# Kernel tuning notes

Hardware: AMD Instinct MI355X
Metric: run time of the kernel (lower is better)

## Reference

```python
import jax, jax.numpy as jnp
import numpy as np

B, MN, GN, ME, GE = 1, 40962, 65160, 327660, 163848
MEMB = EEMB = 256
H1, H2 = 512, 64
EPS = 1e-5


def setup_inputs() -> dict:
    key = jax.random.key(0)
    ks = jax.random.split(key, 16)
    s = 0.05
    return {
        "gx": jax.random.normal(ks[0], (B, GN, MEMB), jnp.float32),
        "mx": jax.random.normal(ks[1], (B, MN, MEMB), jnp.float32),
        "me_i": jax.random.randint(ks[2], (2, ME), 0, MN),
        "me_x": jax.random.normal(ks[3], (B, ME, EEMB), jnp.float32),
        "g2me_i": jax.random.randint(ks[4], (2, GE), 0, MN),
        "g2me_x": jax.random.normal(ks[5], (B, GE, EEMB), jnp.float32),
        "m2ge_i": jax.random.randint(ks[6], (2, GE), 0, MN),
        "m2ge_x": jax.random.normal(ks[7], (B, GE, EEMB), jnp.float32),
        # learned params (Linear stored as [in, out]; y = x @ W + b, math-equivalent to torch)
        "W1": jax.random.normal(ks[8], (2 * MEMB + EEMB, H1), jnp.float32) * s,
        "b1": jnp.zeros((H1,), jnp.float32),
        "W2": jax.random.normal(ks[9], (H1, H2), jnp.float32) * s,
        "b2": jnp.zeros((H2,), jnp.float32),
        "W3": jax.random.normal(ks[10], (H2, EEMB), jnp.float32) * s,
        "b3": jnp.zeros((EEMB,), jnp.float32),
        # LayerNorm([m_enum, eemb]) -> elementwise affine over last two dims
        "ln_w": jnp.ones((ME, EEMB), jnp.float32),
        "ln_b": jnp.zeros((ME, EEMB), jnp.float32),
    }


def reference(gx, mx, me_i, me_x, g2me_i, g2me_x, m2ge_i, m2ge_x,
              W1, b1, W2, b2, W3, b3, ln_w, ln_b):
    row, col = me_i[0], me_i[1]
    # gather sender/receiver mesh-node features per edge: [B, ME, 2*MEMB+EEMB]
    h = jnp.concatenate([mx[:, row], mx[:, col], me_x], axis=-1)
    h = jax.nn.silu(h @ W1 + b1)
    h = jax.nn.silu(h @ W2 + b2)
    h = h @ W3 + b3
    # LayerNorm over the last TWO dims (m_enum, eemb), as nn.LayerNorm([m_enum, eemb])
    mean = jnp.mean(h, axis=(-2, -1), keepdims=True)
    var = jnp.var(h, axis=(-2, -1), keepdims=True)
    h = (h - mean) * jax.lax.rsqrt(var + EPS) * ln_w + ln_b
    me_x_new = me_x + h
    return (gx, mx, me_i, me_x_new, g2me_i, g2me_x, m2ge_i, m2ge_x)
```

## Files before the change

### kernel.cpp

```cpp
#include <hip/hip_runtime.h>
#include <hip/hip_bf16.h>

typedef unsigned short u16;
typedef unsigned int u32;
typedef __attribute__((ext_vector_type(8))) short bfrag8;
typedef __attribute__((ext_vector_type(4))) float f32x4;

#define ME_N 327660
#define MEMB_N 256
#define H1_N 512
#define H2_N 64
#define EEMB_N 256
#define LN_EPS 1e-5f
#define NBLK 5120

static __device__ __forceinline__ u16 f2bf(float f) {
  __hip_bfloat16 h = __float2bfloat16(f);
  return *reinterpret_cast<u16*>(&h);
}
static __device__ __forceinline__ float bf2f(u16 u) {
  union { u32 i; float f; } x; x.i = ((u32)u) << 16; return x.f;
}
static __device__ __forceinline__ u32 pack2(float a, float b) {
  return (u32)f2bf(a) | ((u32)f2bf(b) << 16);
}
static __device__ __forceinline__ float silu_f(float x) {
  return x / (1.0f + __expf(-x));
}
static __device__ __forceinline__ void gload_lds16(const void* g, void* l) {
  __builtin_amdgcn_global_load_lds(
      (const __attribute__((address_space(1))) void*)g,
      (__attribute__((address_space(3))) void*)l, 16, 0, 0);
}

__global__ void i2f_kernel(const int* __restrict__ src, float* __restrict__ dst, int n) {
  int i = blockIdx.x * 256 + threadIdx.x;
  if (i < n) dst[i] = (float)src[i];
}

__global__ void wconv_kernel(const float* __restrict__ src, u16* __restrict__ dst,
                             int K, int N) {
  int i = blockIdx.x * 256 + threadIdx.x;
  if (i >= K * N) return;
  int n = i / K;
  int k = i - n * K;
  dst[i] = f2bf(src[(size_t)k * N + n]);
}

__launch_bounds__(256, 2)
__global__ void gemm_fused_kernel(const float* __restrict__ mx, const int* __restrict__ me_i,
                                  const float* __restrict__ me_x,
                                  const u16* __restrict__ w1t, const float* __restrict__ b1,
                                  const u16* __restrict__ w2t, const float* __restrict__ b2,
                                  const u16* __restrict__ w3t, const float* __restrict__ b3,
                                  u16* __restrict__ h3, float* __restrict__ partials) {
  __shared__ u16 Alds[64 * 72];
  __shared__ u16 Blds[64 * 520];
  __shared__ float red[8];

  const int t = threadIdx.x;
  const int m0 = blockIdx.x * 64;
  const int lane = t & 63;
  const int wid = t >> 6;
  const int l16 = lane & 15;
  const int k4 = lane >> 4;

  const int arow = t >> 2;
  const int acol = (t & 3) * 16;
  int m_g = m0 + arow; if (m_g > ME_N - 1) m_g = ME_N - 1;
  const float* rp = mx + (size_t)me_i[m_g] * MEMB_N;
  const float* cp = mx + (size_t)me_i[ME_N + m_g] * MEMB_N;
  const float* ep = me_x + (size_t)m_g * EEMB_N;

  const f32x4 zero = {0.f, 0.f, 0.f, 0.f};
  f32x4 acc[4][8];
#pragma unroll
  for (int i = 0; i < 4; ++i)
#pragma unroll
    for (int j = 0; j < 8; ++j) acc[i][j] = zero;

  for (int kc = 0; kc < 12; ++kc) {
    const u16* bsrc = w1t + kc * 64 + (lane & 7) * 8;
#pragma unroll
    for (int q = 0; q < 16; ++q) {
      const int nbase = wid * 128 + q * 8;
      gload_lds16(bsrc + (size_t)(nbase + (lane >> 3)) * 768, &Blds[nbase * 64]);
    }
    const float* p = (kc < 4 ? rp : (kc < 8 ? cp : ep)) + ((kc & 3) * 64 + acol);
    const float4* p4 = reinterpret_cast<const float4*>(p);
    float4 v0 = p4[0], v1 = p4[1], v2 = p4[2], v3 = p4[3];
    uint4 q0, q1;
    q0.x = pack2(v0.x, v0.y); q0.y = pack2(v0.z, v0.w);
    q0.z = pack2(v1.x, v1.y); q0.w = pack2(v1.z, v1.w);
    q1.x = pack2(v2.x, v2.y); q1.y = pack2(v2.z, v2.w);
    q1.z = pack2(v3.x, v3.y); q1.w = pack2(v3.z, v3.w);
    *reinterpret_cast<uint4*>(&Alds[arow * 72 + acol]) = q0;
    *reinterpret_cast<uint4*>(&Alds[arow * 72 + acol + 8]) = q1;
    __syncthreads();
#pragma unroll
    for (int ks = 0; ks < 2; ++ks) {
      bfrag8 a[4], b[8];
#pragma unroll
      for (int i = 0; i < 4; ++i)
        a[i] = *reinterpret_cast<const bfrag8*>(&Alds[(i * 16 + l16) * 72 + ks * 32 + k4 * 8]);
#pragma unroll
      for (int j = 0; j < 8; ++j)
        b[j] = *reinterpret_cast<const bfrag8*>(&Blds[(wid * 128 + j * 16 + l16) * 64 + ks * 32 + k4 * 8]);
#pragma unroll
      for (int i = 0; i < 4; ++i)
#pragma unroll
        for (int j = 0; j < 8; ++j)
          acc[i][j] = __builtin_amdgcn_mfma_f32_16x16x32_bf16(a[i], b[j], acc[i][j], 0, 0, 0);
    }
    __syncthreads();
  }

  float b1v[8];
#pragma unroll
  for (int j = 0; j < 8; ++j) b1v[j] = b1[wid * 128 + j * 16 + l16];
#pragma unroll
  for (int i = 0; i < 4; ++i)
#pragma unroll
    for (int j = 0; j < 8; ++j)
#pragma unroll
      for (int rg = 0; rg < 4; ++rg) {
        float v = silu_f(acc[i][j][rg] + b1v[j]);
        Blds[(i * 16 + k4 * 4 + rg) * 520 + wid * 128 + j * 16 + l16] = f2bf(v);
      }
  __syncthreads();

  const int n2 = wid * 16 + l16;
  bfrag8 w2f[16];
#pragma unroll
  for (int ks = 0; ks < 16; ++ks)
    w2f[ks] = *reinterpret_cast<const bfrag8*>(w2t + (size_t)n2 * 512 + ks * 32 + k4 * 8);
  f32x4 acc2[4];
#pragma unroll
  for (int i = 0; i < 4; ++i) acc2[i] = zero;
#pragma unroll
  for (int ks = 0; ks < 16; ++ks) {
#pragma unroll
    for (int i = 0; i < 4; ++i) {
      bfrag8 a2 = *reinterpret_cast<const bfrag8*>(&Blds[(i * 16 + l16) * 520 + ks * 32 + k4 * 8]);
      acc2[i] = __builtin_amdgcn_mfma_f32_16x16x32_bf16(a2, w2f[ks], acc2[i], 0, 0, 0);
    }
  }
  const float b2v = b2[n2];
#pragma unroll
  for (int i = 0; i < 4; ++i)
#pragma unroll
    for (int rg = 0; rg < 4; ++rg) {
      float v = silu_f(acc2[i][rg] + b2v);
      Alds[(i * 16 + k4 * 4 + rg) * 72 + n2] = f2bf(v);
    }
  __syncthreads();

  bfrag8 w3f[4][2];
#pragma unroll
  for (int j = 0; j < 4; ++j)
#pragma unroll
    for (int ks = 0; ks < 2; ++ks)
      w3f[j][ks] = *reinterpret_cast<const bfrag8*>(
          w3t + (size_t)(wid * 64 + j * 16 + l16) * 64 + ks * 32 + k4 * 8);
  f32x4 acc3[4][4];
#pragma unroll
  for (int i = 0; i < 4; ++i)
#pragma unroll
    for (int j = 0; j < 4; ++j) acc3[i][j] = zero;
#pragma unroll
  for (int ks = 0; ks < 2; ++ks) {
    bfrag8 a3[4];
#pragma unroll
    for (int i = 0; i < 4; ++i)
      a3[i] = *reinterpret_cast<const bfrag8*>(&Alds[(i * 16 + l16) * 72 + ks * 32 + k4 * 8]);
#pragma unroll
    for (int i = 0; i < 4; ++i)
#pragma unroll
      for (int j = 0; j < 4; ++j)
        acc3[i][j] = __builtin_amdgcn_mfma_f32_16x16x32_bf16(a3[i], w3f[j][ks], acc3[i][j], 0, 0, 0);
  }

  float b3v[4];
#pragma unroll
  for (int j = 0; j < 4; ++j) b3v[j] = b3[wid * 64 + j * 16 + l16];
  float lsum = 0.f, lsq = 0.f;
#pragma unroll
  for (int i = 0; i < 4; ++i)
#pragma unroll
    for (int rg = 0; rg < 4; ++rg) {
      int m = m0 + i * 16 + k4 * 4 + rg;
      if (m < ME_N) {
#pragma unroll
        for (int j = 0; j < 4; ++j) {
          float v = acc3[i][j][rg] + b3v[j];
          h3[(size_t)m * EEMB_N + wid * 64 + j * 16 + l16] = f2bf(v);
          lsum += v;
          lsq += v * v;
        }
      }
    }
#pragma unroll
  for (int o = 32; o > 0; o >>= 1) {
    lsum += __shfl_down(lsum, o, 64);
    lsq  += __shfl_down(lsq, o, 64);
  }
  if (lane == 0) { red[wid] = lsum; red[4 + wid] = lsq; }
  __syncthreads();
  if (t == 0) {
    partials[2 * blockIdx.x]     = red[0] + red[1] + red[2] + red[3];
    partials[2 * blockIdx.x + 1] = red[4] + red[5] + red[6] + red[7];
  }
}

__global__ void reduce_kernel(const float* __restrict__ partials, int n,
                              float* __restrict__ stats) {
  __shared__ float s1[256], s2[256];
  float a = 0.f, b = 0.f;
  for (int i = threadIdx.x; i < n; i += 256) { a += partials[2 * i]; b += partials[2 * i + 1]; }
  s1[threadIdx.x] = a; s2[threadIdx.x] = b;
  __syncthreads();
  for (int off = 128; off > 0; off >>= 1) {
    if ((int)threadIdx.x < off) {
      s1[threadIdx.x] += s1[threadIdx.x + off];
      s2[threadIdx.x] += s2[threadIdx.x + off];
    }
    __syncthreads();
  }
  if (threadIdx.x == 0) {
    double cnt = (double)ME_N * (double)EEMB_N;
    double mean = (double)s1[0] / cnt;
    double var = (double)s2[0] / cnt - mean * mean;
    stats[0] = (float)mean;
    stats[1] = (float)(1.0 / sqrt(var + (double)LN_EPS));
  }
}

__launch_bounds__(256)
__global__ void final_kernel(const u16* __restrict__ h3, const float* __restrict__ me_x,
                             const float* __restrict__ ln_w, const float* __restrict__ ln_b,
                             const float* __restrict__ stats, float* __restrict__ out) {
  const size_t total = (size_t)ME_N * EEMB_N;
  size_t i = ((size_t)blockIdx.x * 256 + threadIdx.x) * 8;
  if (i >= total) return;
  const float mean = stats[0], inv = stats[1];
  uint4 hv = *reinterpret_cast<const uint4*>(h3 + i);
  float h[8];
  h[0] = bf2f((u16)(hv.x & 0xffff)); h[1] = bf2f((u16)(hv.x >> 16));
  h[2] = bf2f((u16)(hv.y & 0xffff)); h[3] = bf2f((u16)(hv.y >> 16));
  h[4] = bf2f((u16)(hv.z & 0xffff)); h[5] = bf2f((u16)(hv.z >> 16));
  h[6] = bf2f((u16)(hv.w & 0xffff)); h[7] = bf2f((u16)(hv.w >> 16));
  float4 m0 = reinterpret_cast<const float4*>(me_x + i)[0];
  float4 m1 = reinterpret_cast<const float4*>(me_x + i)[1];
  float4 w0 = reinterpret_cast<const float4*>(ln_w + i)[0];
  float4 w1 = reinterpret_cast<const float4*>(ln_w + i)[1];
  float4 c0 = reinterpret_cast<const float4*>(ln_b + i)[0];
  float4 c1 = reinterpret_cast<const float4*>(ln_b + i)[1];
  float4 o0, o1;
  o0.x = m0.x + (h[0] - mean) * inv * w0.x + c0.x;
  o0.y = m0.y + (h[1] - mean) * inv * w0.y + c0.y;
  o0.z = m0.z + (h[2] - mean) * inv * w0.z + c0.z;
  o0.w = m0.w + (h[3] - mean) * inv * w0.w + c0.w;
  o1.x = m1.x + (h[4] - mean) * inv * w1.x + c1.x;
  o1.y = m1.y + (h[5] - mean) * inv * w1.y + c1.y;
  o1.z = m1.z + (h[6] - mean) * inv * w1.z + c1.z;
  o1.w = m1.w + (h[7] - mean) * inv * w1.w + c1.w;
  reinterpret_cast<float4*>(out + i)[0] = o0;
  reinterpret_cast<float4*>(out + i)[1] = o1;
}

extern "C" void kernel_launch(void* const* d_in, const int* in_sizes, int n_in,
                              void* d_out, int out_size, void* d_ws, size_t ws_size,
                              hipStream_t stream) {
  const float* mx   = (const float*)d_in[1];
  const int*   me_i = (const int*)d_in[2];
  const float* me_x = (const float*)d_in[3];
  const float* W1 = (const float*)d_in[8];
  const float* b1 = (const float*)d_in[9];
  const float* W2 = (const float*)d_in[10];
  const float* b2 = (const float*)d_in[11];
  const float* W3 = (const float*)d_in[12];
  const float* b3 = (const float*)d_in[13];
  const float* ln_w = (const float*)d_in[14];
  const float* ln_b = (const float*)d_in[15];

  char* ws = (char*)d_ws;
  u16* w1t = (u16*)(ws + 0);
  u16* w2t = (u16*)(ws + 786432);
  u16* w3t = (u16*)(ws + 851968);
  u16* h3  = (u16*)(ws + 884736);
  float* partials = (float*)(ws + 884736 + 167761920);
  float* stats    = (float*)(ws + 884736 + 167761920 + 40960);

  size_t off[8]; size_t a = 0;
  for (int i = 0; i < 8; ++i) { off[i] = a; a += (size_t)in_sizes[i]; }

  for (int i = 0; i < 8; ++i) {
    if (i == 3) continue;
    if (i == 2 || i == 4 || i == 6) {
      int n = in_sizes[i];
      i2f_kernel<<<(n + 255) / 256, 256, 0, stream>>>(
          (const int*)d_in[i], (float*)d_out + off[i], n);
    } else {
      hipMemcpyAsync((char*)d_out + off[i] * 4, d_in[i], (size_t)in_sizes[i] * 4,
                     hipMemcpyDeviceToDevice, stream);
    }
  }

  wconv_kernel<<<(768 * 512 + 255) / 256, 256, 0, stream>>>(W1, w1t, 768, 512);
  wconv_kernel<<<(512 * 64 + 255) / 256, 256, 0, stream>>>(W2, w2t, 512, 64);
  wconv_kernel<<<(64 * 256 + 255) / 256, 256, 0, stream>>>(W3, w3t, 64, 256);

  gemm_fused_kernel<<<NBLK, 256, 0, stream>>>(mx, me_i, me_x, w1t, b1, w2t, b2,
                                              w3t, b3, h3, partials);
  reduce_kernel<<<1, 256, 0, stream>>>(partials, NBLK, stats);

  const size_t total8 = (size_t)ME_N * EEMB_N / 8;
  final_kernel<<<(int)((total8 + 255) / 256), 256, 0, stream>>>(
      h3, me_x, ln_w, ln_b, stats, (float*)d_out + off[3]);
}
```

Baseline: 974.4 us.

## Pre-convert mesh features to bf16, double-buffer A via async LDS loads, read W1 fragments directly

New measurement: 911.8 us. -6.4%, faster.

```diff
diff --git a/kernel.cpp b/kernel.cpp
--- a/kernel.cpp
+++ b/kernel.cpp
@@ -7,6 +7,7 @@
 typedef __attribute__((ext_vector_type(4))) float f32x4;
 
 #define ME_N 327660
+#define MN_N 40962
 #define MEMB_N 256
 #define H1_N 512
 #define H2_N 64
@@ -36,6 +37,32 @@
 __global__ void i2f_kernel(const int* __restrict__ src, float* __restrict__ dst, int n) {
   int i = blockIdx.x * 256 + threadIdx.x;
   if (i < n) dst[i] = (float)src[i];
+}
+
+__global__ void bfconv_kernel(const float* __restrict__ src, u16* __restrict__ dst, int n) {
+  int i = (blockIdx.x * 256 + threadIdx.x) * 8;
+  if (i >= n) return;
+  float4 v0 = reinterpret_cast<const float4*>(src + i)[0];
+  float4 v1 = reinterpret_cast<const float4*>(src + i)[1];
+  uint4 q;
+  q.x = pack2(v0.x, v0.y); q.y = pack2(v0.z, v0.w);
+  q.z = pack2(v1.x, v1.y); q.w = pack2(v1.z, v1.w);
+  *reinterpret_cast<uint4*>(dst + i) = q;
+}
+
+__global__ void wconv1_kernel(const float* __restrict__ src, u16* __restrict__ dst) {
+  int i = blockIdx.x * 256 + threadIdx.x;
+  if (i >= 512 * 768) return;
+  int e   = i & 7;
+  int l16 = (i >> 3) & 15;
+  int k4  = (i >> 7) & 3;
+  int ks  = (i >> 9) & 1;
+  int rest = i >> 10;
+  int kc = rest % 12;
+  int J  = rest / 12;
+  int n = J * 16 + l16;
+  int k = kc * 64 + ks * 32 + k4 * 8 + e;
+  dst[i] = f2bf(src[(size_t)k * 512 + n]);
 }
 
 __global__ void wconv_kernel(const float* __restrict__ src, u16* __restrict__ dst,
@@ -48,15 +75,17 @@
 }
 
 __launch_bounds__(256, 2)
-__global__ void gemm_fused_kernel(const float* __restrict__ mx, const int* __restrict__ me_i,
+__global__ void gemm_fused_kernel(const u16* __restrict__ mxb, const int* __restrict__ me_i,
                                   const float* __restrict__ me_x,
-                                  const u16* __restrict__ w1t, const float* __restrict__ b1,
+                                  const u16* __restrict__ w1f, const float* __restrict__ b1,
                                   const u16* __restrict__ w2t, const float* __restrict__ b2,
                                   const u16* __restrict__ w3t, const float* __restrict__ b3,
                                   u16* __restrict__ h3, float* __restrict__ partials) {
-  __shared__ u16 Alds[64 * 72];
-  __shared__ u16 Blds[64 * 520];
+  __shared__ u16 S[64 * 520 + 64 * 72];
   __shared__ float red[8];
+  u16* Abuf = S;
+  u16* h1T  = S;
+  u16* h2T  = S + 64 * 520;
 
   const int t = threadIdx.x;
   const int m0 = blockIdx.x * 64;
@@ -65,12 +94,21 @@
   const int l16 = lane & 15;
   const int k4 = lane >> 4;
 
-  const int arow = t >> 2;
-  const int acol = (t & 3) * 16;
-  int m_g = m0 + arow; if (m_g > ME_N - 1) m_g = ME_N - 1;
-  const float* rp = mx + (size_t)me_i[m_g] * MEMB_N;
-  const float* cp = mx + (size_t)me_i[ME_N + m_g] * MEMB_N;
-  const float* ep = me_x + (size_t)m_g * EEMB_N;
+  const int c0 = wid * 128 + lane;
+  const int c1 = c0 + 64;
+  const int r0 = c0 >> 3, r1 = c1 >> 3;
+  const int e0s = ((c0 & 7) ^ (r0 & 7)) * 8;
+  const int e1s = ((c1 & 7) ^ (r1 & 7)) * 8;
+  const int mg0 = min(m0 + r0, ME_N - 1);
+  const int mg1 = min(m0 + r1, ME_N - 1);
+  const u16* row0r = mxb + (size_t)me_i[mg0] * MEMB_N;
+  const u16* row0c = mxb + (size_t)me_i[ME_N + mg0] * MEMB_N;
+  const u16* row1r = mxb + (size_t)me_i[mg1] * MEMB_N;
+  const u16* row1c = mxb + (size_t)me_i[ME_N + mg1] * MEMB_N;
+  const int rr = t >> 2, g = t & 3;
+  const float* pe = me_x + (size_t)min(m0 + rr, ME_N - 1) * EEMB_N;
+  const int E0 = (g * 16) ^ ((rr & 7) * 8);
+  const int E1 = (g * 16 + 8) ^ ((rr & 7) * 8);
 
   const f32x4 zero = {0.f, 0.f, 0.f, 0.f};
   f32x4 acc[4][8];
@@ -79,38 +117,55 @@
 #pragma unroll
     for (int j = 0; j < 8; ++j) acc[i][j] = zero;
 
+  auto stage_A = [&](int kcn) {
+    if (kcn < 8) {
+      const u16* s0 = (kcn < 4 ? row0r : row0c) + ((kcn & 3) * 64 + e0s);
+      const u16* s1 = (kcn < 4 ? row1r : row1c) + ((kcn & 3) * 64 + e1s);
+      u16* lb = Abuf + (kcn & 1) * 4096 + wid * 1024;
+      gload_lds16(s0, lb);
+      gload_lds16(s1, lb + 512);
+    } else {
+      const float4* p4 = reinterpret_cast<const float4*>(pe + (kcn - 8) * 64 + g * 16);
+      float4 v0 = p4[0], v1 = p4[1], v2 = p4[2], v3 = p4[3];
+      uint4 qa, qb;
+      qa.x = pack2(v0.x, v0.y); qa.y = pack2(v0.z, v0.w);
+      qa.z = pack2(v1.x, v1.y); qa.w = pack2(v1.z, v1.w);
+      qb.x = pack2(v2.x, v2.y); qb.y = pack2(v2.z, v2.w);
+      qb.z = pack2(v3.x, v3.y); qb.w = pack2(v3.z, v3.w);
+      u16* d = Abuf + (kcn & 1) * 4096 + rr * 64;
+      *reinterpret_cast<uint4*>(d + E0) = qa;
+      *reinterpret_cast<uint4*>(d + E1) = qb;
+    }
+  };
+
+  stage_A(0);
+  __syncthreads();
+
   for (int kc = 0; kc < 12; ++kc) {
-    const u16* bsrc = w1t + kc * 64 + (lane & 7) * 8;
-#pragma unroll
-    for (int q = 0; q < 16; ++q) {
-      const int nbase = wid * 128 + q * 8;
-      gload_lds16(bsrc + (size_t)(nbase + (lane >> 3)) * 768, &Blds[nbase * 64]);
-    }
-    const float* p = (kc < 4 ? rp : (kc < 8 ? cp : ep)) + ((kc & 3) * 64 + acol);
-    const float4* p4 = reinterpret_cast<const float4*>(p);
-    float4 v0 = p4[0], v1 = p4[1], v2 = p4[2], v3 = p4[3];
-    uint4 q0, q1;
-    q0.x = pack2(v0.x, v0.y); q0.y = pack2(v0.z, v0.w);
-    q0.z = pack2(v1.x, v1.y); q0.w = pack2(v1.z, v1.w);
-    q1.x = pack2(v2.x, v2.y); q1.y = pack2(v2.z, v2.w);
-    q1.z = pack2(v3.x, v3.y); q1.w = pack2(v3.z, v3.w);
-    *reinterpret_cast<uint4*>(&Alds[arow * 72 + acol]) = q0;
-    *reinterpret_cast<uint4*>(&Alds[arow * 72 + acol + 8]) = q1;
-    __syncthreads();
+    if (kc < 11) stage_A(kc + 1);
+    bfrag8 bfr[2][8];
+    {
+      const u16* bb = w1f + (size_t)kc * 1024 + k4 * 128 + l16 * 8;
+      const size_t woff = (size_t)(wid * 8) * 12288;
+#pragma unroll
+      for (int ks = 0; ks < 2; ++ks)
+#pragma unroll
+        for (int j = 0; j < 8; ++j)
+          bfr[ks][j] = *reinterpret_cast<const bfrag8*>(bb + woff + (size_t)j * 12288 + ks * 512);
+    }
+    const u16* ab = Abuf + (kc & 1) * 4096;
 #pragma unroll
     for (int ks = 0; ks < 2; ++ks) {
-      bfrag8 a[4], b[8];
+      bfrag8 a[4];
 #pragma unroll
       for (int i = 0; i < 4; ++i)
-        a[i] = *reinterpret_cast<const bfrag8*>(&Alds[(i * 16 + l16) * 72 + ks * 32 + k4 * 8]);
-#pragma unroll
-      for (int j = 0; j < 8; ++j)
-        b[j] = *reinterpret_cast<const bfrag8*>(&Blds[(wid * 128 + j * 16 + l16) * 64 + ks * 32 + k4 * 8]);
+        a[i] = *reinterpret_cast<const bfrag8*>(
+            &ab[(i * 16 + l16) * 64 + ((ks * 32 + k4 * 8) ^ ((l16 & 7) * 8))]);
 #pragma unroll
       for (int i = 0; i < 4; ++i)
 #pragma unroll
         for (int j = 0; j < 8; ++j)
-          acc[i][j] = __builtin_amdgcn_mfma_f32_16x16x32_bf16(a[i], b[j], acc[i][j], 0, 0, 0);
+          acc[i][j] = __builtin_amdgcn_mfma_f32_16x16x32_bf16(a[i], bfr[ks][j], acc[i][j], 0, 0, 0);
     }
     __syncthreads();
   }
@@ -125,7 +180,7 @@
 #pragma unroll
       for (int rg = 0; rg < 4; ++rg) {
         float v = silu_f(acc[i][j][rg] + b1v[j]);
-        Blds[(i * 16 + k4 * 4 + rg) * 520 + wid * 128 + j * 16 + l16] = f2bf(v);
+        h1T[(i * 16 + k4 * 4 + rg) * 520 + wid * 128 + j * 16 + l16] = f2bf(v);
       }
   __syncthreads();
 
@@ -141,7 +196,7 @@
   for (int ks = 0; ks < 16; ++ks) {
 #pragma unroll
     for (int i = 0; i < 4; ++i) {
-      bfrag8 a2 = *reinterpret_cast<const bfrag8*>(&Blds[(i * 16 + l16) * 520 + ks * 32 + k4 * 8]);
+      bfrag8 a2 = *reinterpret_cast<const bfrag8*>(&h1T[(i * 16 + l16) * 520 + ks * 32 + k4 * 8]);
       acc2[i] = __builtin_amdgcn_mfma_f32_16x16x32_bf16(a2, w2f[ks], acc2[i], 0, 0, 0);
     }
   }
@@ -151,7 +206,7 @@
 #pragma unroll
     for (int rg = 0; rg < 4; ++rg) {
       float v = silu_f(acc2[i][rg] + b2v);
-      Alds[(i * 16 + k4 * 4 + rg) * 72 + n2] = f2bf(v);
+      h2T[(i * 16 + k4 * 4 + rg) * 72 + n2] = f2bf(v);
     }
   __syncthreads();
 
@@ -172,7 +227,7 @@
     bfrag8 a3[4];
 #pragma unroll
     for (int i = 0; i < 4; ++i)
-      a3[i] = *reinterpret_cast<const bfrag8*>(&Alds[(i * 16 + l16) * 72 + ks * 32 + k4 * 8]);
+      a3[i] = *reinterpret_cast<const bfrag8*>(&h2T[(i * 16 + l16) * 72 + ks * 32 + k4 * 8]);
 #pragma unroll
     for (int i = 0; i < 4; ++i)
 #pragma unroll
@@ -284,12 +339,13 @@
   const float* ln_b = (const float*)d_in[15];
 
   char* ws = (char*)d_ws;
-  u16* w1t = (u16*)(ws + 0);
+  u16* w1f = (u16*)(ws + 0);
   u16* w2t = (u16*)(ws + 786432);
   u16* w3t = (u16*)(ws + 851968);
-  u16* h3  = (u16*)(ws + 884736);
-  float* partials = (float*)(ws + 884736 + 167761920);
-  float* stats    = (float*)(ws + 884736 + 167761920 + 40960);
+  u16* mxb = (u16*)(ws + 884736);
+  u16* h3  = (u16*)(ws + 21857280);
+  float* partials = (float*)(ws + 189619200);
+  float* stats    = (float*)(ws + 189660160);
 
   size_t off[8]; size_t a = 0;
   for (int i = 0; i < 8; ++i) { off[i] = a; a += (size_t)in_sizes[i]; }
@@ -306,11 +362,15 @@
     }
   }
 
-  wconv_kernel<<<(768 * 512 + 255) / 256, 256, 0, stream>>>(W1, w1t, 768, 512);
+  wconv1_kernel<<<(512 * 768 + 255) / 256, 256, 0, stream>>>(W1, w1f);
   wconv_kernel<<<(512 * 64 + 255) / 256, 256, 0, stream>>>(W2, w2t, 512, 64);
   wconv_kernel<<<(64 * 256 + 255) / 256, 256, 0, stream>>>(W3, w3t, 64, 256);
-
-  gemm_fused_kernel<<<NBLK, 256, 0, stream>>>(mx, me_i, me_x, w1t, b1, w2t, b2,
+  {
+    int n = MN_N * MEMB_N;
+    bfconv_kernel<<<(n / 8 + 255) / 256, 256, 0, stream>>>(mx, mxb, n);
+  }
+
+  gemm_fused_kernel<<<NBLK, 256, 0, stream>>>(mxb, me_i, me_x, w1f, b1, w2t, b2,
                                               w3t, b3, h3, partials);
   reduce_kernel<<<1, 256, 0, stream>>>(partials, NBLK, stats);
 
```
